# Performance work log

Measured on AMD Instinct MI355X. Metric: run time of the kernel, lower is better.

Reference implementation:

```python
import jax, jax.numpy as jnp
import numpy as np


def _tconv(x, w, b):
    # x: [B,C_in,N,T], w: [C_out,C_in,1,k] -> 'same' padding along T only
    pad = (w.shape[-1] - 1) // 2
    y = jax.lax.conv_general_dilated(x, w, (1, 1), [(0, 0), (pad, pad)],
                                     dimension_numbers=('NCHW', 'OIHW', 'NCHW'))
    return y + b[None, :, None, None]


def _temporal(x, w1, b1, w2, b2, w3, b3):
    # x: [B,T,N,C] -> gated GLU-style temporal conv -> [B,T,N,C_out]
    xc = jnp.transpose(x, (0, 3, 2, 1))  # [B,C,N,T]
    p = _tconv(xc, w1, b1)
    q = jax.nn.sigmoid(_tconv(xc, w2, b2))
    h = jax.nn.relu(p * q + _tconv(xc, w3, b3))
    return jnp.transpose(h, (0, 3, 2, 1))


def _cheb(x, src, dst, wn, W, bias):
    # x: [M,N,C]; scaled Laplacian with lambda_max=2 => L_hat = -D^-1/2 A D^-1/2
    # (diag +1 from L and -1 self-loop fill cancel exactly, as in PyG ChebConv)
    N = x.shape[1]

    def spmv(v):
        msgs = v[:, src, :] * wn[None, :, None]
        return jnp.zeros_like(v).at[:, dst, :].add(msgs)

    Tx0 = x
    out = jnp.einsum('mnc,cd->mnd', Tx0, W[0])
    Tx1 = spmv(Tx0)
    out = out + jnp.einsum('mnc,cd->mnd', Tx1, W[1])
    Txp, Txpp = Tx1, Tx0
    for k in range(2, W.shape[0]):
        Txk = 2.0 * spmv(Txp) - Txpp
        out = out + jnp.einsum('mnc,cd->mnd', Txk, W[k])
        Txpp, Txp = Txp, Txk
    return out + bias


def _bn_train(out, gamma, beta, eps=1e-5):
    # BatchNorm2d in training mode (batch stats, biased variance) over [B,C,N,T]
    ob = jnp.transpose(out, (0, 3, 2, 1))
    mu = jnp.mean(ob, axis=(0, 2, 3), keepdims=True)
    var = jnp.mean((ob - mu) ** 2, axis=(0, 2, 3), keepdims=True)
    ob = (ob - mu) * jax.lax.rsqrt(var + eps)
    ob = ob * gamma[None, :, None, None] + beta[None, :, None, None]
    return jnp.transpose(ob, (0, 3, 2, 1))


def setup_inputs():
    B, T, N, Cin, H, k, K, E = 16, 12, 4096, 2, 64, 3, 3, 65536
    ks = jax.random.split(jax.random.key(0), 20)
    sc = 0.1
    return {
        'x': jax.random.normal(ks[0], (B, T, N, Cin), jnp.float32),
        'edge_index': jax.random.randint(ks[1], (2, E), 0, N),
        'edge_attr': jax.random.uniform(ks[2], (E,), jnp.float32),
        't1_w1': jax.random.normal(ks[3], (H, Cin, 1, k), jnp.float32) * sc,
        't1_b1': jnp.zeros((H,), jnp.float32),
        't1_w2': jax.random.normal(ks[4], (H, Cin, 1, k), jnp.float32) * sc,
        't1_b2': jnp.zeros((H,), jnp.float32),
        't1_w3': jax.random.normal(ks[5], (H, Cin, 1, k), jnp.float32) * sc,
        't1_b3': jnp.zeros((H,), jnp.float32),
        'cheb_W': jax.random.normal(ks[6], (K, H, H), jnp.float32) * sc,
        'cheb_b': jnp.zeros((H,), jnp.float32),
        't2_w1': jax.random.normal(ks[7], (H, H, 1, k), jnp.float32) * sc,
        't2_b1': jnp.zeros((H,), jnp.float32),
        't2_w2': jax.random.normal(ks[8], (H, H, 1, k), jnp.float32) * sc,
        't2_b2': jnp.zeros((H,), jnp.float32),
        't2_w3': jax.random.normal(ks[9], (H, H, 1, k), jnp.float32) * sc,
        't2_b3': jnp.zeros((H,), jnp.float32),
        'bn_g': jnp.ones((H,), jnp.float32),
        'bn_b': jnp.zeros((H,), jnp.float32),
    }


def reference(x, edge_index, edge_attr,
              t1_w1, t1_b1, t1_w2, t1_b2, t1_w3, t1_b3,
              cheb_W, cheb_b,
              t2_w1, t2_b1, t2_w2, t2_b2, t2_w3, t2_b3,
              bn_g, bn_b):
    t1 = _temporal(x, t1_w1, t1_b1, t1_w2, t1_b2, t1_w3, t1_b3)  # [B,T,N,H]
    B, T, N, C = t1.shape
    src, dst = edge_index[0], edge_index[1]
    # sym normalization: deg from source scatter; -D^-1/2 w D^-1/2 edge weights
    deg = jnp.zeros((N,), t1.dtype).at[src].add(edge_attr)
    safe = jnp.where(deg > 0, deg, 1.0)
    dis = jnp.where(deg > 0, jax.lax.rsqrt(safe), 0.0)
    wn = -dis[src] * edge_attr * dis[dst]
    g = _cheb(t1.reshape(B * T, N, C), src, dst, wn, cheb_W, cheb_b)
    g = jax.nn.relu(g).reshape(B, T, N, C)
    out = _temporal(g, t2_w1, t2_b1, t2_w2, t2_b2, t2_w3, t2_b3)
    return _bn_train(out, bn_g, bn_b)
```

## Files before the change

kernel.cpp:

```cpp
#include <hip/hip_runtime.h>
#include <stdint.h>

#define BB 16
#define TT 12
#define NN 4096
#define HH 64
#define EE 65536
#define MM (BB*TT)
#define ROWS (MM*NN)
#define TOT (ROWS*HH)
#define NBUCKET 256
#define T2_GRID 2048
#define T2_NT 6

typedef __attribute__((ext_vector_type(8))) __bf16 bf16x8;
typedef __attribute__((ext_vector_type(8))) unsigned short us8;
typedef __attribute__((ext_vector_type(4))) float f32x4;

__device__ __forceinline__ unsigned short f2bf(float f){
  unsigned u = __builtin_bit_cast(unsigned, f);
  u += 0x7fffu + ((u >> 16) & 1u);
  return (unsigned short)(u >> 16);
}
__device__ __forceinline__ float bf2f(unsigned short s){
  unsigned u = ((unsigned)s) << 16;
  return __builtin_bit_cast(float, u);
}
__device__ __forceinline__ bf16x8 ldbf8(const unsigned short* p){
  us8 u = *reinterpret_cast<const us8*>(p);
  return __builtin_bit_cast(bf16x8, u);
}


__global__ void k_deg_cnt(const int* __restrict__ src, const int* __restrict__ dst,
                          const float* __restrict__ attr,
                          float* __restrict__ deg, int* __restrict__ cnt){
  int e = blockIdx.x * 256 + threadIdx.x;
  if (e < EE){
    atomicAdd(&deg[src[e]], attr[e]);
    atomicAdd(&cnt[dst[e]], 1);
  }
}

__global__ void k_wn(const int* __restrict__ src, const int* __restrict__ dst,
                     const float* __restrict__ attr, const float* __restrict__ deg,
                     float* __restrict__ wn){
  int e = blockIdx.x * 256 + threadIdx.x;
  if (e < EE){
    float ds = deg[src[e]], dd = deg[dst[e]];
    float rs = ds > 0.f ? rsqrtf(ds) : 0.f;
    float rd = dd > 0.f ? rsqrtf(dd) : 0.f;
    wn[e] = -rs * attr[e] * rd;
  }
}

__global__ void k_scan(const int* __restrict__ cnt, int* __restrict__ rowptr,
                       int* __restrict__ fill){
  __shared__ int lds[1024];
  int t = threadIdx.x;
  int c0 = cnt[4*t], c1 = cnt[4*t+1], c2 = cnt[4*t+2], c3 = cnt[4*t+3];
  int s = c0 + c1 + c2 + c3;
  lds[t] = s; __syncthreads();
  for (int off = 1; off < 1024; off <<= 1){
    int v = (t >= off) ? lds[t-off] : 0;
    __syncthreads();
    lds[t] += v;
    __syncthreads();
  }
  int excl = lds[t] - s;
  rowptr[4*t]   = excl;            fill[4*t]   = excl;
  rowptr[4*t+1] = excl + c0;       fill[4*t+1] = excl + c0;
  rowptr[4*t+2] = excl + c0 + c1;  fill[4*t+2] = excl + c0 + c1;
  rowptr[4*t+3] = excl + c0+c1+c2; fill[4*t+3] = excl + c0+c1+c2;
  if (t == 1023) rowptr[4096] = lds[1023];
}

__global__ void k_csr(const int* __restrict__ dst, const int* __restrict__ src,
                      const float* __restrict__ wn, int* __restrict__ fill,
                      int* __restrict__ csrs, float* __restrict__ csrw){
  int e = blockIdx.x * 256 + threadIdx.x;
  if (e < EE){
    int d = dst[e];
    int pos = atomicAdd(&fill[d], 1);
    csrs[pos] = src[e];
    csrw[pos] = wn[e];
  }
}


__global__ void k_wprep(const float* __restrict__ chebW,
                        const float* __restrict__ w1, const float* __restrict__ w2,
                        const float* __restrict__ w3,
                        const float* __restrict__ e1w, const float* __restrict__ e1b,
                        const float* __restrict__ e2w, const float* __restrict__ e2b,
                        const float* __restrict__ e3w, const float* __restrict__ e3b,
                        unsigned short* __restrict__ wfD, unsigned short* __restrict__ wfF,
                        unsigned short* __restrict__ wfE){
  int gt = blockIdx.x * blockDim.x + threadIdx.x;
  int stride = gridDim.x * blockDim.x;
  for (int i = gt; i < 12288; i += stride){
    int kl = i & 31, cc = (i >> 5) & 63, mk = i >> 11;
    int kt = mk & 1, mat = mk >> 1;
    int k = kt * 32 + kl;
    float v;
    if (mat == 0)      v = chebW[k*64 + cc] - chebW[2*4096 + k*64 + cc];
    else if (mat == 1) v = chebW[4096 + k*64 + cc];
    else               v = 2.f * chebW[2*4096 + k*64 + cc];
    wfD[i] = f2bf(v);
  }
  for (int i = gt; i < 36864; i += stride){
    int kl = i & 31, hh = (i >> 5) & 63, ck = i >> 11;
    int kt = ck % 6, conv = ck / 6;
    int k = kt * 32 + kl, dt = k >> 6, ci = k & 63;
    const float* w = (conv == 0) ? w1 : ((conv == 1) ? w2 : w3);
    wfF[i] = f2bf(w[(hh*64 + ci)*3 + dt]);
  }
  for (int i = gt; i < 6144; i += stride){
    int k = i & 31, hh = (i >> 5) & 63, conv = i >> 11;
    const float* w = (conv == 0) ? e1w : ((conv == 1) ? e2w : e3w);
    const float* b = (conv == 0) ? e1b : ((conv == 1) ? e2b : e3b);
    float v = 0.f;
    if (k < 6)       v = w[(hh*2 + (k & 1))*3 + (k >> 1)];
    else if (k == 6) v = b[hh];
    wfE[i] = f2bf(v);
  }
}


__global__ __launch_bounds__(256) void k_temporal1(
    const float* __restrict__ x, const unsigned short* __restrict__ wfE,
    unsigned short* __restrict__ U){
  const int tid = threadIdx.x;
  const int wv = tid >> 6, lane = tid & 63;
  const int lhi = lane >> 4, llo = lane & 15;
  const int blk = blockIdx.x;
  const int bt = blk >> 6, nb = blk & 63;
  const int t = bt - (bt / TT) * TT;

  us8 au = {0,0,0,0,0,0,0,0};
  if (lhi == 0){
    const int n = nb*64 + wv*16 + llo;
    #pragma unroll
    for (int dt = 0; dt < 3; ++dt){
      int tp = t + dt - 1;
      if (tp >= 0 && tp < TT){
        const float2 v = *reinterpret_cast<const float2*>(
            x + ((size_t)(bt + dt - 1) * NN + n) * 2);
        if (dt == 0){ au[0] = f2bf(v.x); au[1] = f2bf(v.y); }
        if (dt == 1){ au[2] = f2bf(v.x); au[3] = f2bf(v.y); }
        if (dt == 2){ au[4] = f2bf(v.x); au[5] = f2bf(v.y); }
      }
    }
    au[6] = 0x3f80;
  }
  const bf16x8 af = __builtin_bit_cast(bf16x8, au);

  const f32x4 z = {0.f, 0.f, 0.f, 0.f};
  f32x4 acc[3][4];
  #pragma unroll
  for (int conv = 0; conv < 3; ++conv)
    #pragma unroll
    for (int ht = 0; ht < 4; ++ht){
      bf16x8 bw = ldbf8(wfE + (size_t)((conv*64) + ht*16 + llo)*32 + lhi*8);
      acc[conv][ht] = __builtin_amdgcn_mfma_f32_16x16x32_bf16(af, bw, z, 0, 0, 0);
    }

  #pragma unroll
  for (int ht = 0; ht < 4; ++ht){
    const int h = ht*16 + llo;
    #pragma unroll
    for (int i = 0; i < 4; ++i){
      float p = acc[0][ht][i];
      float q = acc[1][ht][i];
      float r = acc[2][ht][i];
      float sig = 1.f / (1.f + __expf(-q));
      float o = fmaxf(fmaf(p, sig, r), 0.f);
      const int n = nb*64 + wv*16 + lhi*4 + i;
      U[((size_t)bt * NN + n) * 64 + h] = f2bf(o);
    }
  }
}


template<int PHASE>
__global__ __launch_bounds__(256) void k_spmv(
    const unsigned short* __restrict__ X,
    const int* __restrict__ rowptr,
    const int* __restrict__ csrs, const float* __restrict__ csrw,
    const unsigned short* __restrict__ G0bf,
    unsigned short* __restrict__ Y){
  constexpr int MT = 4;
  constexpr int EU = 8;
  const int nb = gridDim.x;
  int bs = (blockIdx.x & 7) * (nb >> 3) + (blockIdx.x >> 3);
  int wg = bs * 4 + (threadIdx.x >> 6);
  wg = __builtin_amdgcn_readfirstlane(wg);
  const int lane = threadIdx.x & 63;
  const int mg = wg >> 12, n = wg & (NN-1);
  int e0 = __builtin_amdgcn_readfirstlane(rowptr[n]);
  int e1 = __builtin_amdgcn_readfirstlane(rowptr[n+1]);
  const unsigned short* Xb = X + (((size_t)mg * MT) << 12) * 64 + lane;

  float acc[MT];
  #pragma unroll
  for (int j = 0; j < MT; ++j) acc[j] = 0.f;

  for (int e = e0; e < e1; e += EU){
    int ss[EU]; float ww[EU];
    #pragma unroll
    for (int u = 0; u < EU; ++u){
      int ee = e + u;
      bool in = ee < e1;
      ss[u] = csrs[in ? ee : e0];
      ww[u] = in ? csrw[ee] : 0.f;
    }
    unsigned short v[EU][MT];
    #pragma unroll
    for (int u = 0; u < EU; ++u){
      #pragma unroll
      for (int j = 0; j < MT; ++j)
        v[u][j] = Xb[j * (NN*64) + (ss[u] << 6)];
    }
    #pragma unroll
    for (int u = 0; u < EU; ++u)
      #pragma unroll
      for (int j = 0; j < MT; ++j)
        acc[j] = fmaf(ww[u], bf2f(v[u][j]), acc[j]);
  }

  #pragma unroll
  for (int j = 0; j < MT; ++j){
    size_t idx = (((size_t)(mg * MT + j) * NN) + n) * 64 + lane;
    if (PHASE == 1){
      Y[idx] = f2bf(acc[j]);
    } else {
      float gv = bf2f(G0bf[idx]) + acc[j];
      Y[idx] = f2bf(fmaxf(gv, 0.f));
    }
  }
}


__global__ __launch_bounds__(256) void k_cheb_gemm(
    const unsigned short* __restrict__ U, const unsigned short* __restrict__ V,
    const unsigned short* __restrict__ wfD, const float* __restrict__ cheb_b,
    unsigned short* __restrict__ G0bf, unsigned short* __restrict__ P){
  const int tid = threadIdx.x;
  const int wv = tid >> 6, lane = tid & 63;
  const int lhi = lane >> 4, llo = lane & 15;
  const int rbase = blockIdx.x * 64;
  const int c = wv * 16 + llo;

  bf16x8 bA[2], bW1[2], bW2[2];
  #pragma unroll
  for (int kt = 0; kt < 2; ++kt){
    bA[kt]  = ldbf8(wfD + (size_t)((0*2 + kt)*64 + c)*32 + lhi*8);
    bW1[kt] = ldbf8(wfD + (size_t)((1*2 + kt)*64 + c)*32 + lhi*8);
    bW2[kt] = ldbf8(wfD + (size_t)((2*2 + kt)*64 + c)*32 + lhi*8);
  }
  f32x4 z = {0.f, 0.f, 0.f, 0.f};
  f32x4 accG[4], accP[4];
  #pragma unroll
  for (int rt = 0; rt < 4; ++rt){ accG[rt] = z; accP[rt] = z; }

  #pragma unroll
  for (int rt = 0; rt < 4; ++rt){
    const size_t r = (size_t)rbase + rt*16 + llo;
    const unsigned short* up = U + r*64 + lhi*8;
    const unsigned short* vp = V + r*64 + lhi*8;
    #pragma unroll
    for (int kt = 0; kt < 2; ++kt){
      bf16x8 au = ldbf8(up + kt*32);
      bf16x8 av = ldbf8(vp + kt*32);
      accG[rt] = __builtin_amdgcn_mfma_f32_16x16x32_bf16(au, bA[kt],  accG[rt], 0, 0, 0);
      accG[rt] = __builtin_amdgcn_mfma_f32_16x16x32_bf16(av, bW1[kt], accG[rt], 0, 0, 0);
      accP[rt] = __builtin_amdgcn_mfma_f32_16x16x32_bf16(av, bW2[kt], accP[rt], 0, 0, 0);
    }
  }
  __syncthreads();
  float bias = cheb_b[c];
  #pragma unroll
  for (int rt = 0; rt < 4; ++rt){
    #pragma unroll
    for (int i = 0; i < 4; ++i){
      size_t row = (size_t)rbase + rt*16 + lhi*4 + i;
      G0bf[row*64 + c] = f2bf(accG[rt][i] + bias);
      P[row*64 + c]    = f2bf(accP[rt][i]);
    }
  }
}


__device__ __forceinline__ void t2_load(const unsigned short* __restrict__ g,
                                        int tile, int tid, uint4* st){
  const int bt = tile >> 6, nb = tile & 63;
  const int t = bt - (bt / TT) * TT;
  #pragma unroll
  for (int j = 0; j < 6; ++j){
    const int plane = j >> 1;
    const int tp = t + plane - 1;
    const int idx = ((j & 1) << 8) + tid;
    const int row = idx >> 3;
    const int innerb = (idx & 7) * 16;
    if (tp >= 0 && tp < TT){
      const unsigned short* sp = g
          + ((size_t)(bt + plane - 1) * NN + nb*64 + row) * 64
          + ((innerb ^ ((row & 7) << 4)) >> 1);
      st[j] = *reinterpret_cast<const uint4*>(sp);
    } else {
      st[j] = make_uint4(0u, 0u, 0u, 0u);
    }
  }
}

__global__ __launch_bounds__(256, 2) void k_temporal2(
    const unsigned short* __restrict__ g,
    const unsigned short* __restrict__ wfF,
    const float* __restrict__ b1, const float* __restrict__ b2, const float* __restrict__ b3,
    unsigned short* __restrict__ obf, float* __restrict__ bnstat2){
  __shared__ unsigned short smem[2][12288];
  const int tid = threadIdx.x;
  const int wv = tid >> 6, lane = tid & 63;
  const int lhi = lane >> 4, llo = lane & 15;
  const int h = wv * 16 + llo;
  const int h0 = wv * 16 + lhi * 4;

  bf16x8 bw[3][6];
  #pragma unroll
  for (int cv = 0; cv < 3; ++cv)
    #pragma unroll
    for (int kt = 0; kt < 6; ++kt)
      bw[cv][kt] = ldbf8(wfF + (size_t)((cv*6 + kt)*64 + h)*32 + lhi*8);

  const f32x4 vb1 = *reinterpret_cast<const f32x4*>(b1 + h0);
  const f32x4 vb2 = *reinterpret_cast<const f32x4*>(b2 + h0);
  const f32x4 vb3 = *reinterpret_cast<const f32x4*>(b3 + h0);
  const f32x4 z = {0.f, 0.f, 0.f, 0.f};

  uint4 st[6];
  t2_load(g, blockIdx.x, tid, st);
  #pragma unroll
  for (int j = 0; j < 6; ++j)
    *reinterpret_cast<uint4*>(&smem[0][(size_t)(j*256 + tid) * 8]) = st[j];
  __syncthreads();

  int cur = 0;
  for (int it = 0; it < T2_NT; ++it){
    const int tile = blockIdx.x + it * T2_GRID;
    const int bt = tile >> 6, nb = tile & 63;

    if (it + 1 < T2_NT)
      t2_load(g, tile + T2_GRID, tid, st);

    const unsigned short* sb = smem[cur];
    f32x4 acc[3][4];
    #pragma unroll
    for (int cv = 0; cv < 3; ++cv)
      #pragma unroll
      for (int rt = 0; rt < 4; ++rt) acc[cv][rt] = z;

    #pragma unroll
    for (int kt = 0; kt < 6; ++kt){
      const int dt = kt >> 1;
      const int qb = (kt & 1) * 64 + lhi * 16;
      #pragma unroll
      for (int rt = 0; rt < 4; ++rt){
        const int row = rt*16 + llo;
        bf16x8 a = __builtin_bit_cast(bf16x8, *reinterpret_cast<const us8*>(
            sb + dt*4096 + row*64 + ((qb ^ ((row & 7) << 4)) >> 1)));
        acc[0][rt] = __builtin_amdgcn_mfma_f32_16x16x32_bf16(bw[0][kt], a, acc[0][rt], 0, 0, 0);
        acc[1][rt] = __builtin_amdgcn_mfma_f32_16x16x32_bf16(bw[1][kt], a, acc[1][rt], 0, 0, 0);
        acc[2][rt] = __builtin_amdgcn_mfma_f32_16x16x32_bf16(bw[2][kt], a, acc[2][rt], 0, 0, 0);
      }
    }

    f32x4 lsum = z, lsq = z;
    #pragma unroll
    for (int rt = 0; rt < 4; ++rt){
      const int n = nb*64 + rt*16 + llo;
      ushort4 pk;
      unsigned short* pp = reinterpret_cast<unsigned short*>(&pk);
      #pragma unroll
      for (int i = 0; i < 4; ++i){
        float p = acc[0][rt][i] + vb1[i];
        float q = acc[1][rt][i] + vb2[i];
        float r = acc[2][rt][i] + vb3[i];
        float sig = 1.f / (1.f + __expf(-q));
        float o = fmaxf(fmaf(p, sig, r), 0.f);
        pp[i] = f2bf(o);
        lsum[i] += o; lsq[i] = fmaf(o, o, lsq[i]);
      }
      *reinterpret_cast<ushort4*>(&obf[((size_t)bt * NN + n) * 64 + h0]) = pk;
    }
    #pragma unroll
    for (int m = 1; m < 16; m <<= 1){
      #pragma unroll
      for (int i = 0; i < 4; ++i){
        lsum[i] += __shfl_xor(lsum[i], m);
        lsq[i]  += __shfl_xor(lsq[i], m);
      }
    }
    if (llo == 0){
      float* bs = bnstat2 + (size_t)(tile & (NBUCKET-1)) * 128;
      #pragma unroll
      for (int i = 0; i < 4; ++i){
        atomicAdd(&bs[h0 + i], lsum[i]);
        atomicAdd(&bs[64 + h0 + i], lsq[i]);
      }
    }

    if (it + 1 < T2_NT){
      #pragma unroll
      for (int j = 0; j < 6; ++j)
        *reinterpret_cast<uint4*>(&smem[cur ^ 1][(size_t)(j*256 + tid) * 8]) = st[j];
      __syncthreads();
      cur ^= 1;
    }
  }
}


__global__ void k_bnfinal(const float* __restrict__ bnstat2, float* __restrict__ bnstat){
  int t = threadIdx.x;
  float s = 0.f;
  for (int b = 0; b < NBUCKET; ++b) s += bnstat2[(size_t)b * 128 + t];
  bnstat[t] = s;
}

__global__ __launch_bounds__(256) void k_bnapply(
    const unsigned short* __restrict__ obf, float* __restrict__ out,
    const float* __restrict__ bnstat,
    const float* __restrict__ gamma, const float* __restrict__ beta){
  __shared__ float ssc[64], sfb[64];
  int tid = threadIdx.x;
  if (tid < 64){
    const float inv = 1.f / (float)ROWS;
    float s = bnstat[tid], q = bnstat[64 + tid];
    float mu = s * inv;
    float var = q * inv - mu * mu;
    if (var < 0.f) var = 0.f;
    float sc = gamma[tid] * rsqrtf(var + 1e-5f);
    ssc[tid] = sc;
    sfb[tid] = beta[tid] - mu * sc;
  }
  __syncthreads();
  const int ngrp = TOT / 8;
  for (int i = blockIdx.x * 256 + tid; i < ngrp; i += gridDim.x * 256){
    us8 v = *reinterpret_cast<const us8*>(obf + (size_t)i * 8);
    const int c0 = (i * 8) & 63;
    f32x4 lo, hi;
    #pragma unroll
    for (int j = 0; j < 4; ++j)
      lo[j] = fmaf(bf2f(v[j]), ssc[c0 + j], sfb[c0 + j]);
    #pragma unroll
    for (int j = 0; j < 4; ++j)
      hi[j] = fmaf(bf2f(v[4 + j]), ssc[c0 + 4 + j], sfb[c0 + 4 + j]);
    *reinterpret_cast<f32x4*>(out + (size_t)i * 8)     = lo;
    *reinterpret_cast<f32x4*>(out + (size_t)i * 8 + 4) = hi;
  }
}


extern "C" void kernel_launch(void* const* d_in, const int* in_sizes, int n_in,
                              void* d_out, int out_size, void* d_ws, size_t ws_size,
                              hipStream_t stream){
  const float* x     = (const float*)d_in[0];
  const int*   ei    = (const int*)d_in[1];
  const float* attr  = (const float*)d_in[2];
  const float* t1w1  = (const float*)d_in[3];
  const float* t1b1  = (const float*)d_in[4];
  const float* t1w2  = (const float*)d_in[5];
  const float* t1b2  = (const float*)d_in[6];
  const float* t1w3  = (const float*)d_in[7];
  const float* t1b3  = (const float*)d_in[8];
  const float* chebW = (const float*)d_in[9];
  const float* chebB = (const float*)d_in[10];
  const float* t2w1  = (const float*)d_in[11];
  const float* t2b1  = (const float*)d_in[12];
  const float* t2w2  = (const float*)d_in[13];
  const float* t2b2  = (const float*)d_in[14];
  const float* t2w3  = (const float*)d_in[15];
  const float* t2b3  = (const float*)d_in[16];
  const float* bng   = (const float*)d_in[17];
  const float* bnb   = (const float*)d_in[18];
  const int* src = ei;
  const int* dst = ei + EE;

  const size_t SZ_U = (size_t)ROWS * 64 * 2;
  char* ws = (char*)d_ws;
  unsigned short* U = (unsigned short*)ws;
  unsigned short* V = (unsigned short*)(ws + SZ_U);
  size_t off = 2 * SZ_U;
  float* deg    = (float*)(ws + off); off += 4096 * 4;
  int*   cnt    = (int*)(ws + off);   off += 4096 * 4;
  int*   rowptr = (int*)(ws + off);   off += 4128 * 4;
  int*   fill   = (int*)(ws + off);   off += 4096 * 4;
  float* wn     = (float*)(ws + off); off += EE * 4;
  int*   csrs   = (int*)(ws + off);   off += EE * 4;
  float* csrw   = (float*)(ws + off); off += EE * 4;
  unsigned short* wfD = (unsigned short*)(ws + off); off += 12288 * 2;
  unsigned short* wfF = (unsigned short*)(ws + off); off += 36864 * 2;
  unsigned short* wfE = (unsigned short*)(ws + off); off += 6144 * 2;
  float* bnstat = (float*)(ws + off); off += 128 * 4;
  float* bnstat2 = (float*)(ws + off); off += NBUCKET * 128 * 4;

  unsigned short* G0bf = (unsigned short*)d_out;

  hipMemsetAsync(deg, 0, 4096 * 4, stream);
  hipMemsetAsync(cnt, 0, 4096 * 4, stream);
  hipMemsetAsync(bnstat2, 0, NBUCKET * 128 * 4, stream);

  k_deg_cnt<<<EE/256, 256, 0, stream>>>(src, dst, attr, deg, cnt);
  k_wn<<<EE/256, 256, 0, stream>>>(src, dst, attr, deg, wn);
  k_scan<<<1, 1024, 0, stream>>>(cnt, rowptr, fill);
  k_csr<<<EE/256, 256, 0, stream>>>(dst, src, wn, fill, csrs, csrw);
  k_wprep<<<64, 256, 0, stream>>>(chebW, t2w1, t2w2, t2w3,
                                  t1w1, t1b1, t1w2, t1b2, t1w3, t1b3,
                                  wfD, wfF, wfE);

  k_temporal1<<<ROWS/64, 256, 0, stream>>>(x, wfE, U);
  k_spmv<1><<<(MM/4)*NN/4, 256, 0, stream>>>(U, rowptr, csrs, csrw, (const unsigned short*)nullptr, V);
  k_cheb_gemm<<<ROWS/64, 256, 0, stream>>>(U, V, wfD, chebB, G0bf, U );
  k_spmv<2><<<(MM/4)*NN/4, 256, 0, stream>>>(U , rowptr, csrs, csrw, G0bf, V );
  k_temporal2<<<T2_GRID, 256, 0, stream>>>(V , wfF, t2b1, t2b2, t2b3, U , bnstat2);
  k_bnfinal<<<1, 128, 0, stream>>>(bnstat2, bnstat);
  k_bnapply<<<2048, 256, 0, stream>>>(U, (float*)d_out, bnstat, bng, bnb);
}
```

Measured before the change: 678.0 us.

## Switch intermediate activations to node-major layout for contiguous SpMV gathers

Intermediate activations are stored as [node][bt][channel] instead of [bt][node][channel], so each neighbour row gathered in the SpMV is one contiguous 12288-element block. Each lane now loads four consecutive bf16 values with a single 8-byte load covering four bt rows, replacing four scattered 2-byte loads per edge. The temporal producer and the temporal2 loader are updated to the new indexing. The risk is less coalesced writes and reads in the temporal kernels, which now stride by MM*64 across nodes.

```diff
diff --git a/kernel.cpp b/kernel.cpp
--- a/kernel.cpp
+++ b/kernel.cpp
@@ -26,6 +26,8 @@
   unsigned u = ((unsigned)s) << 16;
   return __builtin_bit_cast(float, u);
 }
+__device__ __forceinline__ float lo2f(unsigned v){ return __builtin_bit_cast(float, v << 16); }
+__device__ __forceinline__ float hi2f(unsigned v){ return __builtin_bit_cast(float, v & 0xffff0000u); }
 __device__ __forceinline__ bf16x8 ldbf8(const unsigned short* p){
   us8 u = *reinterpret_cast<const us8*>(p);
   return __builtin_bit_cast(bf16x8, u);
@@ -176,7 +178,7 @@
       float sig = 1.f / (1.f + __expf(-q));
       float o = fmaxf(fmaf(p, sig, r), 0.f);
       const int n = nb*64 + wv*16 + lhi*4 + i;
-      U[((size_t)bt * NN + n) * 64 + h] = f2bf(o);
+      U[((size_t)n * MM + bt) * 64 + h] = f2bf(o);
     }
   }
 }
@@ -189,7 +191,6 @@
     const int* __restrict__ csrs, const float* __restrict__ csrw,
     const unsigned short* __restrict__ G0bf,
     unsigned short* __restrict__ Y){
-  constexpr int MT = 4;
   constexpr int EU = 8;
   const int nb = gridDim.x;
   int bs = (blockIdx.x & 7) * (nb >> 3) + (blockIdx.x >> 3);
@@ -197,13 +198,12 @@
   wg = __builtin_amdgcn_readfirstlane(wg);
   const int lane = threadIdx.x & 63;
   const int mg = wg >> 12, n = wg & (NN-1);
-  int e0 = __builtin_amdgcn_readfirstlane(rowptr[n]);
-  int e1 = __builtin_amdgcn_readfirstlane(rowptr[n+1]);
-  const unsigned short* Xb = X + (((size_t)mg * MT) << 12) * 64 + lane;
-
-  float acc[MT];
-  #pragma unroll
-  for (int j = 0; j < MT; ++j) acc[j] = 0.f;
+  const int e0 = __builtin_amdgcn_readfirstlane(rowptr[n]);
+  const int e1 = __builtin_amdgcn_readfirstlane(rowptr[n+1]);
+  const unsigned short* Xmg = X + (size_t)mg * 256;
+  const int loff = lane * 4;
+
+  float a0 = 0.f, a1 = 0.f, a2 = 0.f, a3 = 0.f;
 
   for (int e = e0; e < e1; e += EU){
     int ss[EU]; float ww[EU];
@@ -211,33 +211,37 @@
     for (int u = 0; u < EU; ++u){
       int ee = e + u;
       bool in = ee < e1;
-      ss[u] = csrs[in ? ee : e0];
+      ss[u] = __builtin_amdgcn_readfirstlane(csrs[in ? ee : e0]);
       ww[u] = in ? csrw[ee] : 0.f;
     }
-    unsigned short v[EU][MT];
+    uint2 d[EU];
     #pragma unroll
     for (int u = 0; u < EU; ++u){
-      #pragma unroll
-      for (int j = 0; j < MT; ++j)
-        v[u][j] = Xb[j * (NN*64) + (ss[u] << 6)];
-    }
-    #pragma unroll
-    for (int u = 0; u < EU; ++u)
-      #pragma unroll
-      for (int j = 0; j < MT; ++j)
-        acc[j] = fmaf(ww[u], bf2f(v[u][j]), acc[j]);
-  }
-
-  #pragma unroll
-  for (int j = 0; j < MT; ++j){
-    size_t idx = (((size_t)(mg * MT + j) * NN) + n) * 64 + lane;
-    if (PHASE == 1){
-      Y[idx] = f2bf(acc[j]);
-    } else {
-      float gv = bf2f(G0bf[idx]) + acc[j];
-      Y[idx] = f2bf(fmaxf(gv, 0.f));
-    }
-  }
+      const unsigned short* rp = Xmg + (size_t)ss[u] * 12288;
+      d[u] = *reinterpret_cast<const uint2*>(rp + loff);
+    }
+    #pragma unroll
+    for (int u = 0; u < EU; ++u){
+      const float w = ww[u];
+      a0 = fmaf(w, lo2f(d[u].x), a0);
+      a1 = fmaf(w, hi2f(d[u].x), a1);
+      a2 = fmaf(w, lo2f(d[u].y), a2);
+      a3 = fmaf(w, hi2f(d[u].y), a3);
+    }
+  }
+
+  const size_t oidx = (size_t)n * 12288 + mg * 256 + loff;
+  if (PHASE == 2){
+    uint2 gd = *reinterpret_cast<const uint2*>(G0bf + oidx);
+    a0 = fmaxf(a0 + lo2f(gd.x), 0.f);
+    a1 = fmaxf(a1 + hi2f(gd.x), 0.f);
+    a2 = fmaxf(a2 + lo2f(gd.y), 0.f);
+    a3 = fmaxf(a3 + hi2f(gd.y), 0.f);
+  }
+  uint2 o;
+  o.x = (unsigned)f2bf(a0) | ((unsigned)f2bf(a1) << 16);
+  o.y = (unsigned)f2bf(a2) | ((unsigned)f2bf(a3) << 16);
+  *reinterpret_cast<uint2*>(Y + oidx) = o;
 }
 
 
@@ -304,7 +308,7 @@
     const int innerb = (idx & 7) * 16;
     if (tp >= 0 && tp < TT){
       const unsigned short* sp = g
-          + ((size_t)(bt + plane - 1) * NN + nb*64 + row) * 64
+          + ((size_t)(nb*64 + row) * MM + (bt + plane - 1)) * 64
           + ((innerb ^ ((row & 7) << 4)) >> 1);
       st[j] = *reinterpret_cast<const uint4*>(sp);
     } else {
```

New measurement: 655.5 us. -3.3%, faster.
